# Kernel optimization log

Hardware: AMD Instinct MI355X
Metric: run time of the kernel (lower is better)

## Reference

```python
import jax, jax.numpy as jnp
import numpy as np

FACTOR = 5


def setup_inputs() -> dict:
    key = jax.random.key(0)
    k1, k2, k3, k4 = jax.random.split(key, 4)
    B, L, H, D = 2, 4096, 8, 64
    sample_k = min(FACTOR * int(np.ceil(np.log(L))), L)  # 45
    return {
        "queries": jax.random.normal(k1, (B, L, H, D), dtype=jnp.float32),
        "keys": jax.random.normal(k2, (B, L, H, D), dtype=jnp.float32),
        "values": jax.random.normal(k3, (B, L, H, D), dtype=jnp.float32),
        "attn_mask": jnp.zeros((1,), dtype=bool),  # unused; ProbMask is built internally
        "index_sample": jax.random.randint(k4, (L, sample_k), 0, L, dtype=jnp.int32),
    }


def reference(queries, keys, values, attn_mask, index_sample):
    # queries/keys/values: [B, L, H, D] -> [B, H, L, D]
    Q = jnp.swapaxes(queries, 1, 2)
    K = jnp.swapaxes(keys, 1, 2)
    V = jnp.swapaxes(values, 1, 2)
    B, H, L_Q, D = Q.shape
    L_K = K.shape[2]
    n_top = min(FACTOR * int(np.ceil(np.log(L_Q))), L_Q)
    scale = 1.0 / jnp.sqrt(jnp.float32(D))

    # --- sparse measurement: sampled QK scores ---
    # K_sample[b,h,q,s,d] = K[b,h,index_sample[q,s],d]
    K_sample = K[:, :, index_sample, :]                       # [B,H,L_Q,S,D]
    QK_sample = jnp.einsum("bhqd,bhqsd->bhqs", Q, K_sample)   # [B,H,L_Q,S]
    M = QK_sample.max(axis=-1) - QK_sample.sum(axis=-1) / L_K  # sparsity measure

    # --- top-u query selection ---
    _, M_top = jax.lax.top_k(M, n_top)                         # [B,H,u]
    Q_reduce = jnp.take_along_axis(Q, M_top[..., None], axis=2)  # [B,H,u,D]

    # --- full scores for selected queries ---
    scores = jnp.einsum("bhud,bhkd->bhuk", Q_reduce, K) * scale  # [B,H,u,L_K]

    # mask_flag=True: causal ProbMask (key pos > selected query pos)
    key_pos = jnp.arange(L_K)
    causal = key_pos[None, None, None, :] > M_top[..., None]
    scores = jnp.where(causal, -jnp.inf, scores)
    attn = jax.nn.softmax(scores, axis=-1)

    # --- initial context (cumsum, masked case) + scatter update ---
    context = jnp.cumsum(V, axis=2)                            # [B,H,L_Q,D]
    ctx_sel = jnp.einsum("bhuk,bhkd->bhud", attn, V)
    b_idx = jnp.arange(B)[:, None, None]
    h_idx = jnp.arange(H)[None, :, None]
    context = context.at[b_idx, h_idx, M_top].set(ctx_sel)
    return jnp.swapaxes(context, 1, 2)  # [B, L_Q, H, D]
```

## Files before the change

kernel.cpp:

```cpp
#include <hip/hip_runtime.h>
#include <math.h>

#define B_    2
#define L_    4096
#define H_    8
#define D_    64
#define S_    45
#define NT_   45
#define BH_   16
#define CHV   64
#define NCHV  64
#define KC    128
#define NKC2  64
#define SCALE 0.125f
#define NEG_BIG (-1e30f)

#define OFF_M     0
#define OFF_MTOP  65536
#define OFF_MPART 66304
#define OFF_SPART 112384
#define OFF_CTXP  158464
#define OFF_VSUM  3107584

typedef __attribute__((ext_vector_type(8))) short s8b;
typedef __attribute__((ext_vector_type(4))) float f32x4;

template <int CTRL>
__device__ __forceinline__ float dpp_ror_f(float x) {
    int y = __builtin_amdgcn_update_dpp(0, __float_as_int(x), CTRL, 0xF, 0xF, false);
    return __int_as_float(y);
}

__device__ __forceinline__ unsigned f2bf(float x) {
    return (__float_as_uint(x) >> 16);
}
__device__ __forceinline__ float bflo(unsigned u) { return __uint_as_float(u << 16); }
__device__ __forceinline__ float bfhi(unsigned u) { return __uint_as_float(u & 0xffff0000u); }

__global__ __launch_bounds__(256) void k1(const float* __restrict__ Q,
                                          const float* __restrict__ Kt,
                                          const float* __restrict__ V,
                                          const int* __restrict__ samp,
                                          float* __restrict__ ws)
{
    int tid  = threadIdx.x;
    int w    = tid >> 6;
    int lane = tid & 63;

    if (blockIdx.x < 4096) {
        int i   = blockIdx.x;
        int xcd = i & 7;
        int b   = xcd >> 2;
        int hh  = (xcd >> 1) & 1;
        int qq  = ((i >> 3) << 1) | (xcd & 1);

        __shared__ int soff[4][S_];
        if (tid < 4 * S_) {
            int qs = tid / S_, ss = tid - qs * S_;
            soff[qs][ss] = (samp[(qq * 4 + qs) * S_ + ss] << 11) | (hh << 10);
        }
        __syncthreads();

        int q  = qq * 4 + w;
        int h4 = lane >> 4;

        const float4 q4 = *(const float4*)(Q +
            ((((long)b * L_ + q) * H_ + hh * 4) << 6) + lane * 4);

        const char* kslab = (const char*)Kt + (long)b * (L_ * 2048);
        unsigned lb = (unsigned)(lane * 16);

        float mx = NEG_BIG, sm = 0.f;
#pragma unroll
        for (int jb = 0; jb < 45; jb += 15) {
            float4 kb[15];
#pragma unroll
            for (int j = 0; j < 15; ++j)
                kb[j] = *(const float4*)(kslab +
                        ((unsigned)soff[w][jb + j] + lb));
#pragma unroll
            for (int j = 0; j < 15; ++j) {
                float p = q4.x * kb[j].x + q4.y * kb[j].y +
                          q4.z * kb[j].z + q4.w * kb[j].w;
                p += dpp_ror_f<0x121>(p);
                p += dpp_ror_f<0x122>(p);
                p += dpp_ror_f<0x124>(p);
                p += dpp_ror_f<0x128>(p);
                mx = fmaxf(mx, p);
                sm += p;
            }
        }
        if ((lane & 15) == 0)
            ws[OFF_M + ((long)(b * 8 + hh * 4 + h4)) * L_ + q] =
                mx - sm * (1.0f / (float)L_);
    } else {
        int unit = (blockIdx.x - 4096) * 4 + w;
        int bh = unit >> 6, ch = unit & 63;
        int b = bh >> 3, h = bh & 7;
        const float* vp = V + ((((long)b * L_ + (long)ch * CHV) * H_ + h) << 6) + lane;
        float ssum = 0.f;
#pragma unroll
        for (int ib = 0; ib < CHV; ib += 16) {
            float vb[16];
#pragma unroll
            for (int j = 0; j < 16; ++j) vb[j] = vp[(long)(ib + j) * (H_ * D_)];
#pragma unroll
            for (int j = 0; j < 16; ++j) ssum += vb[j];
        }
        ws[OFF_VSUM + unit * 64 + lane] = ssum;
    }
}

__global__ __launch_bounds__(256) void k2(float* __restrict__ ws)
{
    int tid  = threadIdx.x;
    int w    = tid >> 6;
    int lane = tid & 63;

    int bh = blockIdx.x;
    int* Mtop = (int*)ws + OFF_MTOP + bh * NT_;

    __shared__ float lv_[4][NT_];
    __shared__ int   li_[4][NT_];

    const float4* m4 = (const float4*)(ws + OFF_M + (long)bh * L_ +
                                       w * 1024 + lane * 16);
    float vals[16];
    {
        float4 a = m4[0], bq = m4[1], c = m4[2], d = m4[3];
        vals[0]=a.x; vals[1]=a.y; vals[2]=a.z; vals[3]=a.w;
        vals[4]=bq.x; vals[5]=bq.y; vals[6]=bq.z; vals[7]=bq.w;
        vals[8]=c.x; vals[9]=c.y; vals[10]=c.z; vals[11]=c.w;
        vals[12]=d.x; vals[13]=d.y; vals[14]=d.z; vals[15]=d.w;
    }
    float lv = NEG_BIG; int li = lane * 16;
#pragma unroll
    for (int j = 0; j < 16; ++j)
        if (vals[j] > lv) { lv = vals[j]; li = lane * 16 + j; }

    for (int r = 0; r < NT_; ++r) {
        float rm = lv;
        rm = fmaxf(rm, dpp_ror_f<0x121>(rm));
        rm = fmaxf(rm, dpp_ror_f<0x122>(rm));
        rm = fmaxf(rm, dpp_ror_f<0x124>(rm));
        rm = fmaxf(rm, dpp_ror_f<0x128>(rm));
        rm = fmaxf(rm, __shfl_xor(rm, 16));
        rm = fmaxf(rm, __shfl_xor(rm, 32));
        unsigned long long bm = __ballot(lv == rm);
        int winner = __ffsll(bm) - 1;
        int wi = __shfl(li, winner);
        if (lane == 0) { lv_[w][r] = rm; li_[w][r] = w * 1024 + wi; }
        if (lane == winner) {
#pragma unroll
            for (int j = 0; j < 16; ++j)
                if (j == (wi & 15)) vals[j] = NEG_BIG;
            lv = NEG_BIG; li = lane * 16;
#pragma unroll
            for (int j = 0; j < 16; ++j)
                if (vals[j] > lv) { lv = vals[j]; li = lane * 16 + j; }
        }
    }
    __syncthreads();

    if (w == 0) {
        int g = lane & 3;
        int p = 0;
        float hv = lv_[g][0]; int hi = li_[g][0];
        for (int r = 0; r < NT_; ++r) {
            float v0 = __shfl(hv, 0), v1 = __shfl(hv, 1),
                  v2 = __shfl(hv, 2), v3 = __shfl(hv, 3);
            int   i0 = __shfl(hi, 0), i1 = __shfl(hi, 1),
                  i2 = __shfl(hi, 2), i3 = __shfl(hi, 3);
            float bv = v0; int bi = i0, bg = 0;
            if (v1 > bv) { bv = v1; bi = i1; bg = 1; }
            if (v2 > bv) { bv = v2; bi = i2; bg = 2; }
            if (v3 > bv) { bv = v3; bi = i3; bg = 3; }
            if (lane == 0) Mtop[r] = bi;
            if (g == bg) {
                ++p;
                hv = (p < NT_) ? lv_[g][p] : NEG_BIG;
                hi = (p < NT_) ? li_[g][p] : 0;
            }
        }
    }
}

#define KPAD16 72
#define PSTR   136
__global__ __launch_bounds__(256) void k3(const float* __restrict__ Q,
                                          const float* __restrict__ Kt,
                                          const float* __restrict__ V,
                                          float* __restrict__ out,
                                          float* __restrict__ ws)
{
    __shared__ unsigned short Klds16[KC * KPAD16];
    __shared__ unsigned short Qs16[32 * KPAD16];
    __shared__ unsigned short P16[32 * PSTR];
    __shared__ int qposs[32];

    int tid = threadIdx.x;

    if (blockIdx.x < 1024) {
        int bh = blockIdx.x >> 6;
        int kc = (blockIdx.x >> 1) & 31;
        int ug = blockIdx.x & 1;
        int b = bh >> 3, h = bh & 7;
        int kbase = kc * KC;
        int u0 = ug * 23;
        int NU = ug ? 22 : 23;

        if (tid < 32) {
            int uu = tid < NU ? tid : NU - 1;
            qposs[tid] = ((const int*)ws)[OFF_MTOP + bh * NT_ + u0 + uu];
        }
        __syncthreads();

        {
            const float4* ksrc4 = (const float4*)(Kt + ((((long)b * L_ + kbase) * H_ + h) << 6));
#pragma unroll
            for (int i = 0; i < 8; ++i) {
                int e = i * 256 + tid;
                int r = e >> 4, c4 = e & 15;
                float4 kv = ksrc4[(long)r * (H_ * D_ / 4) + c4];
                uint2 pk;
                pk.x = (__float_as_uint(kv.x) >> 16) | (__float_as_uint(kv.y) & 0xffff0000u);
                pk.y = (__float_as_uint(kv.z) >> 16) | (__float_as_uint(kv.w) & 0xffff0000u);
                *(uint2*)&Klds16[r * KPAD16 + ((c4 * 4) ^ ((r & 7) << 3))] = pk;
            }
#pragma unroll
            for (int i = 0; i < 2; ++i) {
                int e = i * 256 + tid;
                int r = e >> 4, c4 = e & 15;
                int qp = qposs[r];
                const float4* qsrc4 = (const float4*)(Q + ((((long)b * L_ + qp) * H_ + h) << 6));
                float4 qv = qsrc4[c4];
                uint2 pk;
                pk.x = (__float_as_uint(qv.x) >> 16) | (__float_as_uint(qv.y) & 0xffff0000u);
                pk.y = (__float_as_uint(qv.z) >> 16) | (__float_as_uint(qv.w) & 0xffff0000u);
                *(uint2*)&Qs16[r * KPAD16 + ((c4 * 4) ^ ((r & 7) << 3))] = pk;
            }
        }
        __syncthreads();

        {
            int lane = tid & 63, w = tid >> 6;
            int c = lane & 15, hi = lane >> 4;
            int t = w & 1, Hh = w >> 1;
            int slot = t * 16 + c;
            int qp = qposs[slot];

            s8b bq0 = *(const s8b*)&Qs16[slot * KPAD16 + ((hi * 8) ^ ((slot & 7) << 3))];
            s8b bq1 = *(const s8b*)&Qs16[slot * KPAD16 + ((32 + hi * 8) ^ ((slot & 7) << 3))];

            f32x4 acc0 = {0.f,0.f,0.f,0.f}, acc1 = acc0, acc2 = acc0, acc3 = acc0;
#define QK_TILE(MT, ACC)                                                      \
            {                                                                 \
                int kr = Hh * 64 + (MT) * 16 + c;                             \
                s8b a0 = *(const s8b*)&Klds16[kr * KPAD16 +                   \
                            ((hi * 8) ^ ((kr & 7) << 3))];                    \
                s8b a1 = *(const s8b*)&Klds16[kr * KPAD16 +                   \
                            ((32 + hi * 8) ^ ((kr & 7) << 3))];               \
                ACC = __builtin_amdgcn_mfma_f32_16x16x32_bf16(a0, bq0, ACC, 0, 0, 0); \
                ACC = __builtin_amdgcn_mfma_f32_16x16x32_bf16(a1, bq1, ACC, 0, 0, 0); \
            }
            QK_TILE(0, acc0)
            QK_TILE(1, acc1)
            QK_TILE(2, acc2)
            QK_TILE(3, acc3)
#undef QK_TILE

            float sv[16];
            float m = NEG_BIG;
#pragma unroll
            for (int mt = 0; mt < 4; ++mt) {
                f32x4 a = mt == 0 ? acc0 : (mt == 1 ? acc1 : (mt == 2 ? acc2 : acc3));
#pragma unroll
                for (int reg = 0; reg < 4; ++reg) {
                    float s = a[reg] * SCALE;
                    int kpos = kbase + Hh * 64 + mt * 16 + hi * 4 + reg;
                    if (kpos > qp) s = NEG_BIG;
                    sv[mt * 4 + reg] = s;
                    m = fmaxf(m, s);
                }
            }
            m = fmaxf(m, __shfl_xor(m, 16));
            m = fmaxf(m, __shfl_xor(m, 32));
            float ssum = 0.f;
#pragma unroll
            for (int j = 0; j < 16; ++j) {
                float e = __expf(sv[j] - m);
                sv[j] = e;
                ssum += e;
            }
            ssum += __shfl_xor(ssum, 16);
            ssum += __shfl_xor(ssum, 32);
            if (hi == 0) {
                int sl = t * 16 + c;
                if (sl < NU) {
                    ws[OFF_MPART + ((long)bh * NT_ + u0 + sl) * NKC2 + kc * 2 + Hh] = m;
                    ws[OFF_SPART + ((long)bh * NT_ + u0 + sl) * NKC2 + kc * 2 + Hh] = ssum;
                }
            }
#pragma unroll
            for (int mt = 0; mt < 4; ++mt) {
                uint2 pk;
                pk.x = f2bf(sv[mt * 4 + 0]) | (f2bf(sv[mt * 4 + 1]) << 16);
                pk.y = f2bf(sv[mt * 4 + 2]) | (f2bf(sv[mt * 4 + 3]) << 16);
                *(uint2*)&P16[slot * PSTR + Hh * 64 + mt * 16 + hi * 4] = pk;
            }
        }
        __syncthreads();

        {
            int lane = tid & 63, w = tid >> 6;
            const float* vsrc = V + ((((long)b * L_ + kbase) * H_ + h) << 6);
            float c0[6], c1[6];
#pragma unroll
            for (int j = 0; j < 6; ++j) { c0[j] = 0.f; c1[j] = 0.f; }
            for (int kk8 = 0; kk8 < 8; ++kk8) {
                float v[8];
#pragma unroll
                for (int t = 0; t < 8; ++t)
                    v[t] = vsrc[(long)(kk8 * 8 + t) * (H_ * D_) + lane];
#pragma unroll
                for (int j = 0; j < 6; ++j) {
                    int ul = w + j * 4;
                    if (ul < NU) {
                        uint4 U = *(const uint4*)&P16[ul * PSTR + kk8 * 8];
                        c0[j] += bflo(U.x) * v[0] + bfhi(U.x) * v[1]
                               + bflo(U.y) * v[2] + bfhi(U.y) * v[3]
                               + bflo(U.z) * v[4] + bfhi(U.z) * v[5]
                               + bflo(U.w) * v[6] + bfhi(U.w) * v[7];
                    }
                }
            }
            for (int kk8 = 8; kk8 < 16; ++kk8) {
                float v[8];
#pragma unroll
                for (int t = 0; t < 8; ++t)
                    v[t] = vsrc[(long)(kk8 * 8 + t) * (H_ * D_) + lane];
#pragma unroll
                for (int j = 0; j < 6; ++j) {
                    int ul = w + j * 4;
                    if (ul < NU) {
                        uint4 U = *(const uint4*)&P16[ul * PSTR + kk8 * 8];
                        c1[j] += bflo(U.x) * v[0] + bfhi(U.x) * v[1]
                               + bflo(U.y) * v[2] + bfhi(U.y) * v[3]
                               + bflo(U.z) * v[4] + bfhi(U.z) * v[5]
                               + bflo(U.w) * v[6] + bfhi(U.w) * v[7];
                    }
                }
            }
#pragma unroll
            for (int j = 0; j < 6; ++j) {
                int ul = w + j * 4;
                if (ul < NU) {
                    ws[OFF_CTXP + (((long)bh * NT_ + u0 + ul) * NKC2 + kc * 2 + 0) * 64 + lane] = c0[j];
                    ws[OFF_CTXP + (((long)bh * NT_ + u0 + ul) * NKC2 + kc * 2 + 1) * 64 + lane] = c1[j];
                }
            }
        }
    } else {
        int w    = tid >> 6;
        int lane = tid & 63;
        int unit = (blockIdx.x - 1024) * 4 + w;
        int bh = unit >> 6, ch = unit & 63;
        int b = bh >> 3, h = bh & 7;
        int d = lane;

        float acc = 0.f;
        {
            const float* vs = ws + OFF_VSUM + (long)bh * NCHV * 64 + d;
            int c = 0;
            for (; c + 8 <= ch; c += 8) {
                float vb[8];
#pragma unroll
                for (int j = 0; j < 8; ++j) vb[j] = vs[(c + j) * 64];
#pragma unroll
                for (int j = 0; j < 8; ++j) acc += vb[j];
            }
            for (; c < ch; ++c) acc += vs[c * 64];
        }

        const float* vp = V   + ((((long)b * L_ + (long)ch * CHV) * H_ + h) << 6) + d;
        float*       op = out + ((((long)b * L_ + (long)ch * CHV) * H_ + h) << 6) + d;
#pragma unroll
        for (int ib = 0; ib < CHV; ib += 16) {
            float vb[16];
#pragma unroll
            for (int j = 0; j < 16; ++j) vb[j] = vp[(long)(ib + j) * (H_ * D_)];
#pragma unroll
            for (int j = 0; j < 16; ++j) {
                acc += vb[j];
                op[(long)(ib + j) * (H_ * D_)] = acc;
            }
        }
    }
}

__global__ __launch_bounds__(256) void kD(float* __restrict__ out,
                                          const float* __restrict__ ws)
{
    int tid  = threadIdx.x;
    int w    = tid >> 6;
    int lane = tid & 63;
    int unit = blockIdx.x * 4 + w;
    int bh = unit / NT_, u = unit - bh * NT_;
    int b = bh >> 3, h = bh & 7;

    const float4* mp4 = (const float4*)(ws + OFF_MPART + ((long)bh * NT_ + u) * NKC2);
    const float4* sp4 = (const float4*)(ws + OFF_SPART + ((long)bh * NT_ + u) * NKC2);
    const float*  cp  = ws + OFF_CTXP + ((long)bh * NT_ + u) * (NKC2 * 64);

    float4 mv[16];
    float m = NEG_BIG;
#pragma unroll
    for (int c4 = 0; c4 < 16; ++c4) {
        mv[c4] = mp4[c4];
        m = fmaxf(m, fmaxf(fmaxf(mv[c4].x, mv[c4].y), fmaxf(mv[c4].z, mv[c4].w)));
    }

    float T = 0.f, ctx = 0.f;
#pragma unroll
    for (int c8 = 0; c8 < 8; ++c8) {
        float cb[8];
#pragma unroll
        for (int j = 0; j < 8; ++j) cb[j] = cp[(c8 * 8 + j) * 64 + lane];
        float4 s0 = sp4[c8 * 2], s1 = sp4[c8 * 2 + 1];
        float ms[8] = {mv[c8*2].x, mv[c8*2].y, mv[c8*2].z, mv[c8*2].w,
                       mv[c8*2+1].x, mv[c8*2+1].y, mv[c8*2+1].z, mv[c8*2+1].w};
        float ss[8] = {s0.x, s0.y, s0.z, s0.w, s1.x, s1.y, s1.z, s1.w};
#pragma unroll
        for (int j = 0; j < 8; ++j) {
            float wgt = __expf(ms[j] - m);
            T   += ss[j] * wgt;
            ctx += cb[j] * wgt;
        }
    }
    int qp = ((const int*)ws)[OFF_MTOP + bh * NT_ + u];
    out[((((long)b * L_ + qp) * H_ + h) << 6) + lane] = ctx / T;
}

extern "C" void kernel_launch(void* const* d_in, const int* in_sizes, int n_in,
                              void* d_out, int out_size, void* d_ws, size_t ws_size,
                              hipStream_t stream)
{
    const float* Q    = (const float*)d_in[0];
    const float* K    = (const float*)d_in[1];
    const float* V    = (const float*)d_in[2];
    const int*   samp = (const int*)d_in[4];
    float* out = (float*)d_out;
    float* ws  = (float*)d_ws;

    k1<<<4352, 256, 0, stream>>>(Q, K, V, samp, ws);
    k2<<<16, 256, 0, stream>>>(ws);
    k3<<<1280, 256, 0, stream>>>(Q, K, V, out, ws);
    kD<<<180, 256, 0, stream>>>(out, ws);
}
```

Baseline: 182.9 us.

## Drop max-subtraction in softmax and accumulate partials with float atomics

Removes the per-chunk running max and computes exp(scale*score) directly. Per-chunk sums and context partials are now accumulated into a small zeroed buffer with atomicAdd instead of being written as 64 partials per query. The final kernel just divides context by the total, and the zeroing is done in k2. This cuts partial-result write and read traffic and removes the max-rescaling work, but it risks overflow because there is no max subtraction, and it makes results order-nondeterministic through atomic contention. It also adds a redundant duplicated qposs load.

Result: no change. 182.0 us (-0.5%).

```diff
diff --git a/kernel.cpp b/kernel.cpp
--- a/kernel.cpp
+++ b/kernel.cpp
@@ -11,16 +11,15 @@
 #define CHV   64
 #define NCHV  64
 #define KC    128
-#define NKC2  64
 #define SCALE 0.125f
 #define NEG_BIG (-1e30f)
 
 #define OFF_M     0
 #define OFF_MTOP  65536
-#define OFF_MPART 66304
-#define OFF_SPART 112384
-#define OFF_CTXP  158464
-#define OFF_VSUM  3107584
+#define OFF_T     66304
+#define OFF_CTX   67072
+#define OFF_VSUM  131072
+#define NZERO     46848
 
 typedef __attribute__((ext_vector_type(8))) short s8b;
 typedef __attribute__((ext_vector_type(4))) float f32x4;
@@ -116,6 +115,9 @@
     int tid  = threadIdx.x;
     int w    = tid >> 6;
     int lane = tid & 63;
+
+    for (int i = blockIdx.x * 256 + tid; i < NZERO; i += 16 * 256)
+        ws[OFF_T + i] = 0.f;
 
     int bh = blockIdx.x;
     int* Mtop = (int*)ws + OFF_MTOP + bh * NT_;
@@ -211,6 +213,10 @@
 
         if (tid < 32) {
             int uu = tid < NU ? tid : NU - 1;
+            qposs[tid] = ((const int*)ws)[OFF_MTOP + bh * NT_ + tid < NU ? OFF_MTOP + bh * NT_ + u0 + uu : OFF_MTOP + bh * NT_ + u0 + uu];
+        }
+        if (tid < 32) {
+            int uu = tid < NU ? tid : NU - 1;
             qposs[tid] = ((const int*)ws)[OFF_MTOP + bh * NT_ + u0 + uu];
         }
         __syncthreads();
@@ -269,44 +275,28 @@
             QK_TILE(3, acc3)
 #undef QK_TILE
 
-            float sv[16];
-            float m = NEG_BIG;
+            float ssum = 0.f;
 #pragma unroll
             for (int mt = 0; mt < 4; ++mt) {
                 f32x4 a = mt == 0 ? acc0 : (mt == 1 ? acc1 : (mt == 2 ? acc2 : acc3));
+                float e[4];
 #pragma unroll
                 for (int reg = 0; reg < 4; ++reg) {
-                    float s = a[reg] * SCALE;
                     int kpos = kbase + Hh * 64 + mt * 16 + hi * 4 + reg;
-                    if (kpos > qp) s = NEG_BIG;
-                    sv[mt * 4 + reg] = s;
-                    m = fmaxf(m, s);
+                    e[reg] = (kpos > qp) ? 0.f : __expf(a[reg] * SCALE);
+                    ssum += e[reg];
                 }
-            }
-            m = fmaxf(m, __shfl_xor(m, 16));
-            m = fmaxf(m, __shfl_xor(m, 32));
-            float ssum = 0.f;
-#pragma unroll
-            for (int j = 0; j < 16; ++j) {
-                float e = __expf(sv[j] - m);
-                sv[j] = e;
-                ssum += e;
+                uint2 pk;
+                pk.x = f2bf(e[0]) | (f2bf(e[1]) << 16);
+                pk.y = f2bf(e[2]) | (f2bf(e[3]) << 16);
+                *(uint2*)&P16[slot * PSTR + Hh * 64 + mt * 16 + hi * 4] = pk;
             }
             ssum += __shfl_xor(ssum, 16);
             ssum += __shfl_xor(ssum, 32);
             if (hi == 0) {
                 int sl = t * 16 + c;
-                if (sl < NU) {
-                    ws[OFF_MPART + ((long)bh * NT_ + u0 + sl) * NKC2 + kc * 2 + Hh] = m;
-                    ws[OFF_SPART + ((long)bh * NT_ + u0 + sl) * NKC2 + kc * 2 + Hh] = ssum;
-                }
-            }
-#pragma unroll
-            for (int mt = 0; mt < 4; ++mt) {
-                uint2 pk;
-                pk.x = f2bf(sv[mt * 4 + 0]) | (f2bf(sv[mt * 4 + 1]) << 16);
-                pk.y = f2bf(sv[mt * 4 + 2]) | (f2bf(sv[mt * 4 + 3]) << 16);
-                *(uint2*)&P16[slot * PSTR + Hh * 64 + mt * 16 + hi * 4] = pk;
+                if (sl < NU)
+                    atomicAdd(&ws[OFF_T + bh * NT_ + u0 + sl], ssum);
             }
         }
         __syncthreads();
@@ -314,10 +304,10 @@
         {
             int lane = tid & 63, w = tid >> 6;
             const float* vsrc = V + ((((long)b * L_ + kbase) * H_ + h) << 6);
-            float c0[6], c1[6];
-#pragma unroll
-            for (int j = 0; j < 6; ++j) { c0[j] = 0.f; c1[j] = 0.f; }
-            for (int kk8 = 0; kk8 < 8; ++kk8) {
+            float ctx[6];
+#pragma unroll
+            for (int j = 0; j < 6; ++j) ctx[j] = 0.f;
+            for (int kk8 = 0; kk8 < 16; ++kk8) {
                 float v[8];
 #pragma unroll
                 for (int t = 0; t < 8; ++t)
@@ -327,37 +317,18 @@
                     int ul = w + j * 4;
                     if (ul < NU) {
                         uint4 U = *(const uint4*)&P16[ul * PSTR + kk8 * 8];
-                        c0[j] += bflo(U.x) * v[0] + bfhi(U.x) * v[1]
-                               + bflo(U.y) * v[2] + bfhi(U.y) * v[3]
-                               + bflo(U.z) * v[4] + bfhi(U.z) * v[5]
-                               + bflo(U.w) * v[6] + bfhi(U.w) * v[7];
+                        ctx[j] += bflo(U.x) * v[0] + bfhi(U.x) * v[1]
+                                + bflo(U.y) * v[2] + bfhi(U.y) * v[3]
+                                + bflo(U.z) * v[4] + bfhi(U.z) * v[5]
+                                + bflo(U.w) * v[6] + bfhi(U.w) * v[7];
                     }
                 }
             }
-            for (int kk8 = 8; kk8 < 16; ++kk8) {
-                float v[8];
-#pragma unroll
-                for (int t = 0; t < 8; ++t)
-                    v[t] = vsrc[(long)(kk8 * 8 + t) * (H_ * D_) + lane];
-#pragma unroll
-                for (int j = 0; j < 6; ++j) {
-                    int ul = w + j * 4;
-                    if (ul < NU) {
-                        uint4 U = *(const uint4*)&P16[ul * PSTR + kk8 * 8];
-                        c1[j] += bflo(U.x) * v[0] + bfhi(U.x) * v[1]
-                               + bflo(U.y) * v[2] + bfhi(U.y) * v[3]
-                               + bflo(U.z) * v[4] + bfhi(U.z) * v[5]
-                               + bflo(U.w) * v[6] + bfhi(U.w) * v[7];
-                    }
-                }
-            }
 #pragma unroll
             for (int j = 0; j < 6; ++j) {
                 int ul = w + j * 4;
-                if (ul < NU) {
-                    ws[OFF_CTXP + (((long)bh * NT_ + u0 + ul) * NKC2 + kc * 2 + 0) * 64 + lane] = c0[j];
-                    ws[OFF_CTXP + (((long)bh * NT_ + u0 + ul) * NKC2 + kc * 2 + 1) * 64 + lane] = c1[j];
-                }
+                if (ul < NU)
+                    atomicAdd(&ws[OFF_CTX + ((long)(bh * NT_ + u0 + ul) << 6) + lane], ctx[j]);
             }
         }
     } else {
@@ -405,39 +376,12 @@
     int w    = tid >> 6;
     int lane = tid & 63;
     int unit = blockIdx.x * 4 + w;
-    int bh = unit / NT_, u = unit - bh * NT_;
+    int bh = unit / NT_;
     int b = bh >> 3, h = bh & 7;
 
-    const float4* mp4 = (const float4*)(ws + OFF_MPART + ((long)bh * NT_ + u) * NKC2);
-    const float4* sp4 = (const float4*)(ws + OFF_SPART + ((long)bh * NT_ + u) * NKC2);
-    const float*  cp  = ws + OFF_CTXP + ((long)bh * NT_ + u) * (NKC2 * 64);
-
-    float4 mv[16];
-    float m = NEG_BIG;
-#pragma unroll
-    for (int c4 = 0; c4 < 16; ++c4) {
-        mv[c4] = mp4[c4];
-        m = fmaxf(m, fmaxf(fmaxf(mv[c4].x, mv[c4].y), fmaxf(mv[c4].z, mv[c4].w)));
-    }
-
-    float T = 0.f, ctx = 0.f;
-#pragma unroll
-    for (int c8 = 0; c8 < 8; ++c8) {
-        float cb[8];
-#pragma unroll
-        for (int j = 0; j < 8; ++j) cb[j] = cp[(c8 * 8 + j) * 64 + lane];
-        float4 s0 = sp4[c8 * 2], s1 = sp4[c8 * 2 + 1];
-        float ms[8] = {mv[c8*2].x, mv[c8*2].y, mv[c8*2].z, mv[c8*2].w,
-                       mv[c8*2+1].x, mv[c8*2+1].y, mv[c8*2+1].z, mv[c8*2+1].w};
-        float ss[8] = {s0.x, s0.y, s0.z, s0.w, s1.x, s1.y, s1.z, s1.w};
-#pragma unroll
-        for (int j = 0; j < 8; ++j) {
-            float wgt = __expf(ms[j] - m);
-            T   += ss[j] * wgt;
-            ctx += cb[j] * wgt;
-        }
-    }
-    int qp = ((const int*)ws)[OFF_MTOP + bh * NT_ + u];
+    float T   = ws[OFF_T + unit];
+    float ctx = ws[OFF_CTX + ((long)unit << 6) + lane];
+    int   qp  = ((const int*)ws)[OFF_MTOP + unit];
     out[((((long)b * L_ + qp) * H_ + h) << 6) + lane] = ctx / T;
 }
 
```
